# Optimization experiments

Hardware: AMD Instinct MI355X
Metric: run time of the kernel (lower is better)

Reference implementation:

```python
import jax, jax.numpy as jnp
import numpy as np

B, T, C = 4, 2048, 1024
H, HS = 16, 64  # num_heads, head_size; H*HS == C

def setup_inputs() -> dict:
    key = jax.random.key(0)
    ks = jax.random.split(key, 6)
    s = 0.02
    x = jax.random.normal(ks[0], (B, T, C), dtype=jnp.float32)
    Wq = jax.random.normal(ks[1], (H, C, HS), dtype=jnp.float32) * s
    Wk = jax.random.normal(ks[2], (H, C, HS), dtype=jnp.float32) * s
    Wv = jax.random.normal(ks[3], (H, C, HS), dtype=jnp.float32) * s
    Wproj = jax.random.normal(ks[4], (C, C), dtype=jnp.float32) * s  # applied as out @ Wproj
    bproj = jax.random.normal(ks[5], (C,), dtype=jnp.float32) * s
    return {"x": x, "Wq": Wq, "Wk": Wk, "Wv": Wv, "Wproj": Wproj, "bproj": bproj}

def reference(x, Wq, Wk, Wv, Wproj, bproj):
    Bx, Tx, Cx = x.shape
    scale = Cx ** (-0.5)  # NOTE: original scales by n_embd, not head_size
    q = jnp.einsum('btc,hcd->bhtd', x, Wq)
    k = jnp.einsum('btc,hcd->bhtd', x, Wk)
    v = jnp.einsum('btc,hcd->bhtd', x, Wv)
    wei = jnp.einsum('bhtd,bhsd->bhts', q, k) * scale  # [B,H,T,T]
    causal = jnp.tril(jnp.ones((Tx, Tx), dtype=bool))
    wei = jnp.where(causal, wei, -jnp.inf)
    wei = jax.nn.softmax(wei, axis=-1)
    out = jnp.einsum('bhts,bhsd->bhtd', wei, v)
    out = out.transpose(0, 2, 1, 3).reshape(Bx, Tx, Cx)  # concat heads
    return out @ Wproj + bproj
```

## Files before the change

kernel.cpp:

```cpp
#include <hip/hip_runtime.h>


using u16    = unsigned short;
using u32    = unsigned int;
using bf16x8 = __attribute__((ext_vector_type(8))) short;
using bf16x4 = __attribute__((ext_vector_type(4))) short;
using f32x4  = __attribute__((ext_vector_type(4))) float;

#define MFMA_BF16(a, b, c) __builtin_amdgcn_mfma_f32_16x16x32_bf16((a), (b), (c), 0, 0, 0)

__device__ __forceinline__ f32x4 mfma16(bf16x4 a, bf16x4 b, f32x4 c) {
#if __has_builtin(__builtin_amdgcn_mfma_f32_16x16x16bf16_1k)
    return __builtin_amdgcn_mfma_f32_16x16x16bf16_1k(a, b, c, 0, 0, 0);
#elif __has_builtin(__builtin_amdgcn_mfma_f32_16x16x16_bf16)
    return __builtin_amdgcn_mfma_f32_16x16x16_bf16(a, b, c, 0, 0, 0);
#else
    asm("v_mfma_f32_16x16x16_bf16 %0, %1, %2, %0" : "+v"(c) : "v"(a), "v"(b));
    return c;
#endif
}

__device__ __forceinline__ u16 f2bf(float f) {
    union { float f; unsigned u; } v; v.f = f;
    unsigned u = v.u;
    u += 0x7FFFu + ((u >> 16) & 1u);
    return (u16)(u >> 16);
}
__device__ __forceinline__ short tbf(float f) {
    union { float f; unsigned u; } v; v.f = f;
    return (short)(v.u >> 16);
}
__device__ __forceinline__ float fexp2(float x) {
#if __has_builtin(__builtin_amdgcn_exp2f)
    return __builtin_amdgcn_exp2f(x);
#else
    return exp2f(x);
#endif
}

__device__ __forceinline__ void gl_lds16(const void* g, void* s) {
    __builtin_amdgcn_global_load_lds(
        (__attribute__((address_space(1))) void*)g,
        (__attribute__((address_space(3))) void*)s,
        16, 0, 0);
}

__global__ void cvt_x(const float* __restrict__ x, u16* __restrict__ xb, int n4) {
    int i = blockIdx.x * blockDim.x + threadIdx.x;
    if (i < n4) {
        float4 v = ((const float4*)x)[i];
        ushort4 o;
        o.x = f2bf(v.x); o.y = f2bf(v.y); o.z = f2bf(v.z); o.w = f2bf(v.w);
        ((ushort4*)xb)[i] = o;
    }
}

__global__ void transpose_w(const float* __restrict__ Wq, const float* __restrict__ Wk,
                            const float* __restrict__ Wv, u16* __restrict__ WT) {
    __shared__ float tile[64][65];
    const int tid = threadIdx.x;
    const int c0  = blockIdx.x * 64;
    const int h   = blockIdx.y;
    const int z   = blockIdx.z;
    const float* W = (z == 0 ? Wq : (z == 1 ? Wk : Wv)) + (size_t)h * 1024 * 64;
    u16* out = WT + (size_t)z * 1024 * 1024 + (size_t)h * 64 * 1024;
    #pragma unroll
    for (int i = 0; i < 16; ++i) {
        int idx = i * 256 + tid;
        int r = idx >> 6, d = idx & 63;
        tile[d][r] = W[(size_t)(c0 + r) * 64 + d];
    }
    __syncthreads();
    #pragma unroll
    for (int i = 0; i < 16; ++i) {
        int idx = i * 256 + tid;
        int d = idx >> 6, j = idx & 63;
        out[(size_t)d * 1024 + c0 + j] = f2bf(tile[d][j]);
    }
}

__global__ void transpose_p(const float* __restrict__ Wp, u16* __restrict__ WpT) {
    __shared__ float tile[64][65];
    const int tid = threadIdx.x;
    const int c0  = blockIdx.x * 64;
    const int n0  = blockIdx.y * 64;
    #pragma unroll
    for (int i = 0; i < 16; ++i) {
        int idx = i * 256 + tid;
        int r = idx >> 6, j = idx & 63;
        tile[j][r] = Wp[(size_t)(c0 + r) * 1024 + n0 + j];
    }
    __syncthreads();
    #pragma unroll
    for (int i = 0; i < 16; ++i) {
        int idx = i * 256 + tid;
        int r = idx >> 6, j = idx & 63;
        WpT[(size_t)(n0 + r) * 1024 + c0 + j] = f2bf(tile[r][j]);
    }
}

template <int MODE>
__global__ __launch_bounds__(256, 2)
void gemm_bt(const u16* __restrict__ A, const u16* __restrict__ Bt,
             u16* __restrict__ Oq, u16* __restrict__ Ok, u16* __restrict__ Ov,
             float* __restrict__ Op, const float* __restrict__ bias) {
    constexpr int K = 1024;
    __shared__ u16 SH[2][128 * 32];
    u16* As = SH[0];
    u16* Bs = SH[1];
    const int tid  = threadIdx.x;
    const int w    = tid >> 6;
    const int lane = tid & 63;
    const int quad = lane >> 4;
    const int l16  = lane & 15;
    const int m0   = blockIdx.x * 128;
    const int n0   = blockIdx.y * 128;
    const u16* Bp  = (MODE == 0) ? (Bt + (size_t)blockIdx.z * 1024 * 1024) : Bt;

    const f32x4 zero = {0.f, 0.f, 0.f, 0.f};
    f32x4 acc[4][4];
    #pragma unroll
    for (int i = 0; i < 4; ++i)
        #pragma unroll
        for (int j = 0; j < 4; ++j) acc[i][j] = zero;

    const int wr = (w >> 1) * 64;
    const int wc = (w & 1) * 64;

    for (int k0 = 0; k0 < K; k0 += 32) {
        __syncthreads();
        #pragma unroll
        for (int i = 0; i < 2; ++i) {
            int c = i * 256 + tid;
            int row = c >> 2, ko = (c & 3) * 8;
            gl_lds16(A + (size_t)(m0 + row) * K + (k0 + ko), &As[(i * 256 + w * 64) * 8]);
        }
        #pragma unroll
        for (int i = 0; i < 2; ++i) {
            int c = i * 256 + tid;
            int row = c >> 2, ko = (c & 3) * 8;
            gl_lds16(Bp + (size_t)(n0 + row) * K + (k0 + ko), &Bs[(i * 256 + w * 64) * 8]);
        }
        __syncthreads();
        bf16x8 af[4], bfr[4];
        #pragma unroll
        for (int i = 0; i < 4; ++i)
            af[i] = *(const bf16x8*)&As[(wr + i * 16 + l16) * 32 + quad * 8];
        #pragma unroll
        for (int j = 0; j < 4; ++j)
            bfr[j] = *(const bf16x8*)&Bs[(wc + j * 16 + l16) * 32 + quad * 8];
        #pragma unroll
        for (int i = 0; i < 4; ++i)
            #pragma unroll
            for (int j = 0; j < 4; ++j)
                acc[i][j] = MFMA_BF16(af[i], bfr[j], acc[i][j]);
    }

    if (MODE == 0 && blockIdx.z == 2) {
        u32* buf = (u32*)SH;
        const int bh0 = (m0 >> 11) * 16;
        #pragma unroll
        for (int mh = 0; mh < 2; ++mh) {
            __syncthreads();
            if ((w >> 1) == mh) {
                #pragma unroll
                for (int i = 0; i < 4; ++i)
                    #pragma unroll
                    for (int j = 0; j < 4; ++j)
                        #pragma unroll
                        for (int rp = 0; rp < 2; ++rp) {
                            const int nl = wc + j * 16 + l16;
                            const int t2 = i * 8 + quad * 2 + rp;
                            const u32 lo = f2bf(acc[i][j][2 * rp]);
                            const u32 hi = f2bf(acc[i][j][2 * rp + 1]);
                            buf[nl * 32 + (t2 ^ ((nl & 7) << 2))] = lo | (hi << 16);
                        }
            }
            __syncthreads();
            const int nl = tid >> 1, half = tid & 1;
            const int h = (n0 + nl) >> 6, d = (n0 + nl) & 63;
            u16* orow = Ov + ((size_t)(bh0 + h) * 64 + d) * 2048 + (m0 & 2047) + mh * 64;
            #pragma unroll
            for (int c = 0; c < 4; ++c) {
                const int d2b = half * 16 + c * 4;
                uint4 vv = *(const uint4*)&buf[nl * 32 + (d2b ^ ((nl & 7) << 2))];
                *(uint4*)(orow + d2b * 2) = vv;
            }
        }
    } else {
        #pragma unroll
        for (int i = 0; i < 4; ++i) {
            #pragma unroll
            for (int j = 0; j < 4; ++j) {
                #pragma unroll
                for (int r = 0; r < 4; ++r) {
                    const int m = m0 + wr + i * 16 + quad * 4 + r;
                    const int n = n0 + wc + j * 16 + l16;
                    const float v = acc[i][j][r];
                    if (MODE == 0) {
                        const int b = m >> 11, t = m & 2047;
                        const int h = n >> 6, d = n & 63;
                        const int bh = b * 16 + h;
                        if (blockIdx.z == 0)
                            Oq[((size_t)bh * 2048 + t) * 64 + d] = f2bf(v * 0.0450842203f);
                        else
                            Ok[((size_t)bh * 2048 + t) * 64 + d] = f2bf(v);
                    } else {
                        Op[(size_t)m * 1024 + n] = v + bias[n];
                    }
                }
            }
        }
    }
}

__global__ __launch_bounds__(256, 2)
void attn8(const u16* __restrict__ Q, const u16* __restrict__ Kg,
           const u16* __restrict__ Vt, u16* __restrict__ O) {
    __shared__ __align__(16) u16 Ks[2][2 * 128 * 32];
    __shared__ __align__(16) u16 VF[16 * 128 * 4];
    const int tid  = threadIdx.x;
    const int w    = tid >> 6;
    const int lane = tid & 63;
    const int quad = lane >> 4;
    const int l16  = lane & 15;
    const int bh   = blockIdx.y;
    const u16* Qp = Q  + (size_t)bh * 2048 * 64;
    const u16* Kp = Kg + (size_t)bh * 2048 * 64;
    const u16* Vp = Vt + (size_t)bh * 64 * 2048;
    const int b = bh >> 4, h = bh & 15;
    const float NEG_INF = -__builtin_inff();
    const f32x4 zero = {0.f, 0.f, 0.f, 0.f};
    const short ONE = (short)0x3F80;
    const bf16x4 vones = {ONE, ONE, ONE, ONE};
    const int vd = w * 16 + l16;
    const int ksw = ((l16 >> 3) & 1) << 4;

    #pragma unroll
    for (int ph = 0; ph < 2; ++ph) {
        const int tt = ph ? (int)blockIdx.x : 15 - (int)blockIdx.x;
        const int t0 = tt * 128;
        const int ns = tt + 1;

        bf16x8 bq[2][2];
        #pragma unroll
        for (int tf = 0; tf < 2; ++tf)
            #pragma unroll
            for (int kk = 0; kk < 2; ++kk)
                bq[tf][kk] = *(const bf16x8*)(Qp + (size_t)(t0 + w * 32 + tf * 16 + l16) * 64
                                              + kk * 32 + quad * 8);

        f32x4 oacc[4][2];
        f32x4 lacc[2] = {zero, zero};
        #pragma unroll
        for (int df = 0; df < 4; ++df)
            #pragma unroll
            for (int tf = 0; tf < 2; ++tf) oacc[df][tf] = zero;

        __syncthreads();
        uint4 vr[4];
        #pragma unroll
        for (int i = 0; i < 4; ++i) {
            int c = i * 256 + tid;
            int kk = c >> 9, row = (c >> 2) & 127;
            int q4s = (c & 3) ^ (((row >> 3) & 1) << 1);
            gl_lds16(Kp + (size_t)row * 64 + kk * 32 + q4s * 8,
                     &Ks[0][(size_t)(i * 256 + w * 64) * 8]);
        }
        #pragma unroll
        for (int r = 0; r < 4; ++r)
            vr[r] = *(const uint4*)(Vp + (size_t)vd * 2048 + (r * 4 + quad) * 8);

        for (int it = 0; it < ns; ++it) {
            const int s0 = it * 128;
            const u16* Kc = Ks[it & 1];
            __syncthreads();
            #pragma unroll
            for (int r = 0; r < 4; ++r) {
                const int uA = ((w * 4 + r) * 128) + (quad & 1) * 64 + l16 * 2
                               + ((quad >> 1) & 1);
                *(uint2*)&VF[(size_t)uA * 4]        = make_uint2(vr[r].x, vr[r].y);
                *(uint2*)&VF[(size_t)(uA + 32) * 4] = make_uint2(vr[r].z, vr[r].w);
            }
            __syncthreads();

            if (it + 1 < ns) {
                const int sn = s0 + 128;
                u16* Kn = Ks[(it + 1) & 1];
                #pragma unroll
                for (int i = 0; i < 4; ++i) {
                    int c = i * 256 + tid;
                    int kk = c >> 9, row = (c >> 2) & 127;
                    int q4s = (c & 3) ^ (((row >> 3) & 1) << 1);
                    gl_lds16(Kp + (size_t)(sn + row) * 64 + kk * 32 + q4s * 8,
                             &Kn[(size_t)(i * 256 + w * 64) * 8]);
                }
                #pragma unroll
                for (int r = 0; r < 4; ++r)
                    vr[r] = *(const uint4*)(Vp + (size_t)vd * 2048 + sn + (r * 4 + quad) * 8);
            }

            const bool diag = (it == ns - 1);
            bf16x4 bp[8][2];
            #pragma unroll
            for (int st = 0; st < 8; ++st) {
                const int kbase = (st * 16 + l16) * 32 + quad * 8;
                bf16x8 ak0 = *(const bf16x8*)&Kc[kbase ^ ksw];
                bf16x8 ak1 = *(const bf16x8*)&Kc[(128 * 32) + (kbase ^ ksw)];
                #pragma unroll
                for (int tf = 0; tf < 2; ++tf) {
                    f32x4 s = MFMA_BF16(ak0, bq[tf][0], zero);
                    s = MFMA_BF16(ak1, bq[tf][1], s);
                    if (diag) {
                        #pragma unroll
                        for (int r = 0; r < 4; ++r) {
                            int ss = s0 + st * 16 + quad * 4 + r;
                            int t  = t0 + w * 32 + tf * 16 + l16;
                            if (ss > t) s[r] = NEG_INF;
                        }
                    }
                    float p0 = fexp2(s[0]), p1 = fexp2(s[1]);
                    float p2 = fexp2(s[2]), p3 = fexp2(s[3]);
                    bf16x4 bb; bb[0] = tbf(p0); bb[1] = tbf(p1);
                    bb[2] = tbf(p2); bb[3] = tbf(p3);
                    bp[st][tf] = bb;
                }
            }
            #pragma unroll
            for (int st = 0; st < 8; ++st)
                #pragma unroll
                for (int tf = 0; tf < 2; ++tf)
                    lacc[tf] = mfma16(vones, bp[st][tf], lacc[tf]);
            #pragma unroll
            for (int kcp = 0; kcp < 4; ++kcp)
                #pragma unroll
                for (int df = 0; df < 4; ++df) {
                    bf16x8 av = *(const bf16x8*)&VF[(size_t)(((df * 4 + kcp) * 128)
                                                    + quad * 32 + l16 * 2) * 4];
                    bf16x4 alo = __builtin_shufflevector(av, av, 0, 1, 2, 3);
                    bf16x4 ahi = __builtin_shufflevector(av, av, 4, 5, 6, 7);
                    #pragma unroll
                    for (int tf = 0; tf < 2; ++tf) {
                        oacc[df][tf] = mfma16(alo, bp[2 * kcp][tf], oacc[df][tf]);
                        oacc[df][tf] = mfma16(ahi, bp[2 * kcp + 1][tf], oacc[df][tf]);
                    }
                }
        }

        __syncthreads();
        {
            u32* ob = (u32*)VF;
            const float inv[2] = {1.0f / lacc[0][0], 1.0f / lacc[1][0]};
            #pragma unroll
            for (int df = 0; df < 4; ++df)
                #pragma unroll
                for (int tf = 0; tf < 2; ++tf) {
                    const int tl = w * 32 + tf * 16 + l16;
                    #pragma unroll
                    for (int rp = 0; rp < 2; ++rp) {
                        const u32 lo = f2bf(oacc[df][tf][2 * rp]     * inv[tf]);
                        const u32 hi = f2bf(oacc[df][tf][2 * rp + 1] * inv[tf]);
                        const int d2 = df * 8 + quad * 2 + rp;
                        ob[tl * 32 + (d2 ^ ((tl & 7) << 2))] = lo | (hi << 16);
                    }
                }
            __syncthreads();
            const int tl = tid >> 1, half = tid & 1;
            u16* orow = O + ((size_t)(b * 2048 + t0 + tl)) * 1024 + h * 64;
            #pragma unroll
            for (int c = 0; c < 4; ++c) {
                const int d2b = half * 16 + c * 4;
                uint4 vv = *(const uint4*)&ob[tl * 32 + (d2b ^ ((tl & 7) << 2))];
                *(uint4*)(orow + d2b * 2) = vv;
            }
        }
    }
}

extern "C" void kernel_launch(void* const* d_in, const int* in_sizes, int n_in,
                              void* d_out, int out_size, void* d_ws, size_t ws_size,
                              hipStream_t stream) {
    const float* x  = (const float*)d_in[0];
    const float* Wq = (const float*)d_in[1];
    const float* Wk = (const float*)d_in[2];
    const float* Wv = (const float*)d_in[3];
    const float* Wp = (const float*)d_in[4];
    const float* bp = (const float*)d_in[5];
    float* out = (float*)d_out;

    char* ws = (char*)d_ws;
    u16* Xb  = (u16*)(ws);
    u16* Xo  = (u16*)(ws);
    u16* WT  = (u16*)(ws + (16ull << 20));
    u16* WpT = (u16*)(ws + (22ull << 20));
    u16* Qw  = (u16*)(ws + (24ull << 20));
    u16* Kw  = (u16*)(ws + (40ull << 20));
    u16* Vw  = (u16*)(ws + (56ull << 20));

    cvt_x<<<8192, 256, 0, stream>>>(x, Xb, 8192 * 1024 / 4);
    transpose_w<<<dim3(16, 16, 3), 256, 0, stream>>>(Wq, Wk, Wv, WT);
    transpose_p<<<dim3(16, 16), 256, 0, stream>>>(Wp, WpT);
    gemm_bt<0><<<dim3(64, 8, 3), 256, 0, stream>>>(Xb, WT, Qw, Kw, Vw, nullptr, nullptr);
    attn8<<<dim3(8, 64), 256, 0, stream>>>(Qw, Kw, Vw, Xo);
    gemm_bt<1><<<dim3(64, 8, 1), 256, 0, stream>>>(Xo, WpT, nullptr, nullptr, nullptr, out, bp);
}
```

Measured before the change: 254.6 us.

## Stage V tiles via async global-to-LDS double buffer with XOR swizzle

The attention kernel used to load V into registers and then write it to LDS each iteration, with an extra barrier in between. It now double-buffers V in LDS using the same direct global-to-LDS async loads as K, and reads it back through an XOR swizzle. The K swizzle pattern is also changed to a finer row-pair scheme. This removes the register round-trip and one barrier per iteration, but doubles the V LDS footprint, which may reduce occupancy.

After: 249.8 us. Within noise of the previous version (-1.9%).

```diff
diff --git a/kernel.cpp b/kernel.cpp
--- a/kernel.cpp
+++ b/kernel.cpp
@@ -215,10 +215,10 @@
 }
 
 __global__ __launch_bounds__(256, 2)
-void attn8(const u16* __restrict__ Q, const u16* __restrict__ Kg,
-           const u16* __restrict__ Vt, u16* __restrict__ O) {
+void attn10(const u16* __restrict__ Q, const u16* __restrict__ Kg,
+            const u16* __restrict__ Vt, u16* __restrict__ O) {
     __shared__ __align__(16) u16 Ks[2][2 * 128 * 32];
-    __shared__ __align__(16) u16 VF[16 * 128 * 4];
+    __shared__ __align__(16) u16 Vs[2][64 * 128];
     const int tid  = threadIdx.x;
     const int w    = tid >> 6;
     const int lane = tid & 63;
@@ -233,8 +233,32 @@
     const f32x4 zero = {0.f, 0.f, 0.f, 0.f};
     const short ONE = (short)0x3F80;
     const bf16x4 vones = {ONE, ONE, ONE, ONE};
-    const int vd = w * 16 + l16;
-    const int ksw = ((l16 >> 3) & 1) << 4;
+    const int ksw = ((l16 >> 1) & 3) << 3;
+
+    auto stageK = [&](int sb, u16* dst) {
+        #pragma unroll
+        for (int i = 0; i < 4; ++i) {
+            int c = i * 256 + tid;
+            int kk = c >> 9, row = (c >> 2) & 127;
+            int q4s = (c & 3) ^ ((row >> 1) & 3);
+            gl_lds16(Kp + (size_t)(sb + row) * 64 + kk * 32 + q4s * 8,
+                     dst + (size_t)(i * 256 + w * 64) * 8);
+        }
+    };
+    auto stageV = [&](int sb, u16* dst) {
+        #pragma unroll
+        for (int i = 0; i < 4; ++i) {
+            int j = 4 * w + i;
+            int d = j * 4 + quad;
+            int ci = l16 ^ (d & 7);
+            gl_lds16(Vp + (size_t)d * 2048 + sb + ci * 8, dst + (size_t)j * 512);
+        }
+    };
+    auto ldv = [&](const u16* Vc, int d, int s) -> bf16x4 {
+        int off  = d * 128 + s;
+        int phys = (off & 7) | (((off >> 3) ^ (d & 7)) << 3);
+        return *(const bf16x4*)&Vc[phys];
+    };
 
     #pragma unroll
     for (int ph = 0; ph < 2; ++ph) {
@@ -258,48 +282,19 @@
             for (int tf = 0; tf < 2; ++tf) oacc[df][tf] = zero;
 
         __syncthreads();
-        uint4 vr[4];
-        #pragma unroll
-        for (int i = 0; i < 4; ++i) {
-            int c = i * 256 + tid;
-            int kk = c >> 9, row = (c >> 2) & 127;
-            int q4s = (c & 3) ^ (((row >> 3) & 1) << 1);
-            gl_lds16(Kp + (size_t)row * 64 + kk * 32 + q4s * 8,
-                     &Ks[0][(size_t)(i * 256 + w * 64) * 8]);
-        }
-        #pragma unroll
-        for (int r = 0; r < 4; ++r)
-            vr[r] = *(const uint4*)(Vp + (size_t)vd * 2048 + (r * 4 + quad) * 8);
+        stageK(0, Ks[0]);
+        stageV(0, Vs[0]);
 
         for (int it = 0; it < ns; ++it) {
             const int s0 = it * 128;
+            __syncthreads();
+            if (it + 1 < ns) {
+                stageK(s0 + 128, Ks[(it + 1) & 1]);
+                stageV(s0 + 128, Vs[(it + 1) & 1]);
+            }
+
             const u16* Kc = Ks[it & 1];
-            __syncthreads();
-            #pragma unroll
-            for (int r = 0; r < 4; ++r) {
-                const int uA = ((w * 4 + r) * 128) + (quad & 1) * 64 + l16 * 2
-                               + ((quad >> 1) & 1);
-                *(uint2*)&VF[(size_t)uA * 4]        = make_uint2(vr[r].x, vr[r].y);
-                *(uint2*)&VF[(size_t)(uA + 32) * 4] = make_uint2(vr[r].z, vr[r].w);
-            }
-            __syncthreads();
-
-            if (it + 1 < ns) {
-                const int sn = s0 + 128;
-                u16* Kn = Ks[(it + 1) & 1];
-                #pragma unroll
-                for (int i = 0; i < 4; ++i) {
-                    int c = i * 256 + tid;
-                    int kk = c >> 9, row = (c >> 2) & 127;
-                    int q4s = (c & 3) ^ (((row >> 3) & 1) << 1);
-                    gl_lds16(Kp + (size_t)(sn + row) * 64 + kk * 32 + q4s * 8,
-                             &Kn[(size_t)(i * 256 + w * 64) * 8]);
-                }
-                #pragma unroll
-                for (int r = 0; r < 4; ++r)
-                    vr[r] = *(const uint4*)(Vp + (size_t)vd * 2048 + sn + (r * 4 + quad) * 8);
-            }
-
+            const u16* Vc = Vs[it & 1];
             const bool diag = (it == ns - 1);
             bf16x4 bp[8][2];
             #pragma unroll
@@ -335,10 +330,9 @@
             for (int kcp = 0; kcp < 4; ++kcp)
                 #pragma unroll
                 for (int df = 0; df < 4; ++df) {
-                    bf16x8 av = *(const bf16x8*)&VF[(size_t)(((df * 4 + kcp) * 128)
-                                                    + quad * 32 + l16 * 2) * 4];
-                    bf16x4 alo = __builtin_shufflevector(av, av, 0, 1, 2, 3);
-                    bf16x4 ahi = __builtin_shufflevector(av, av, 4, 5, 6, 7);
+                    const int d = df * 16 + l16;
+                    bf16x4 alo = ldv(Vc, d, kcp * 32 + quad * 4);
+                    bf16x4 ahi = ldv(Vc, d, kcp * 32 + 16 + quad * 4);
                     #pragma unroll
                     for (int tf = 0; tf < 2; ++tf) {
                         oacc[df][tf] = mfma16(alo, bp[2 * kcp][tf], oacc[df][tf]);
@@ -349,7 +343,7 @@
 
         __syncthreads();
         {
-            u32* ob = (u32*)VF;
+            u32* ob = (u32*)Vs;
             const float inv[2] = {1.0f / lacc[0][0], 1.0f / lacc[1][0]};
             #pragma unroll
             for (int df = 0; df < 4; ++df)
@@ -401,6 +395,6 @@
     transpose_w<<<dim3(16, 16, 3), 256, 0, stream>>>(Wq, Wk, Wv, WT);
     transpose_p<<<dim3(16, 16), 256, 0, stream>>>(Wp, WpT);
     gemm_bt<0><<<dim3(64, 8, 3), 256, 0, stream>>>(Xb, WT, Qw, Kw, Vw, nullptr, nullptr);
-    attn8<<<dim3(8, 64), 256, 0, stream>>>(Qw, Kw, Vw, Xo);
+    attn10<<<dim3(8, 64), 256, 0, stream>>>(Qw, Kw, Vw, Xo);
     gemm_bt<1><<<dim3(64, 8, 1), 256, 0, stream>>>(Xo, WpT, nullptr, nullptr, nullptr, out, bp);
 }
```
